# Performance work log

Measured on AMD Instinct MI355X. Metric: run time of the kernel, lower is better.

The kernel has to match this reference:

```python
import jax, jax.numpy as jnp
import numpy as np

LAMBDA_IDENTITY = 1.0
LAMBDA_ATTENTION = 0.5

B, F_FRAMES, N, V = 4, 16, 1024, 4


def setup_inputs() -> dict:
    key = jax.random.key(0)
    k1, k2, k3, k4, k5, k6 = jax.random.split(key, 6)
    refined_points = jax.random.normal(k1, (B, F_FRAMES, N, 3), dtype=jnp.float32)
    gt_points = jax.random.normal(k2, (B, F_FRAMES, N, 3), dtype=jnp.float32)
    visibility = jax.random.randint(k3, (B, F_FRAMES, N), 0, 2, dtype=jnp.int32)
    projection_matrices = jax.random.normal(k4, (V, B, 3, 4), dtype=jnp.float32)
    tracks_2d = jax.random.normal(k5, (V, B, F_FRAMES, N, 2), dtype=jnp.float32)
    correspondence_matrices = jax.random.normal(k6, (V, V, B, N, N), dtype=jnp.float32)
    return {
        'refined_points': refined_points,
        'gt_points': gt_points,
        'visibility': visibility,
        'projection_matrices': projection_matrices,
        'tracks_2d': tracks_2d,
        'correspondence_matrices': correspondence_matrices,
    }


def _reconstruction_loss(pred, gt, visibility):
    mask = (visibility > 0)[..., None]                       # [B,F,N,1]
    se = (pred - gt) ** 2                                    # [B,F,N,3]
    num = jnp.sum(mask) * 3                                  # number of masked scalar elements
    big = jnp.float32(1e30)
    mn = jnp.min(jnp.where(mask, gt, big), axis=(0, 1, 2))   # per-coord min over valid points
    mx = jnp.max(jnp.where(mask, gt, -big), axis=(0, 1, 2))
    scale = jnp.max(mx - mn) + 1e-6
    scale = jnp.where(num > 0, scale, jnp.float32(1.0))
    scale = jax.lax.stop_gradient(scale)
    mse_mean = jnp.sum(jnp.where(mask, se, 0.0)) / jnp.maximum(num, 1)
    return mse_mean / scale ** 2


def _identity_loss(pred, proj, tracks):
    # pred [B,F,N,3], proj [V,B,3,4], tracks [V,B,F,N,2]
    ones = jnp.ones(pred.shape[:-1] + (1,), dtype=pred.dtype)
    homo = jnp.concatenate([pred, ones], axis=-1)            # [B,F,N,4]
    p2h = jnp.einsum('vbij,bfnj->vbfni', proj, homo)         # [V,B,F,N,3]
    p2 = p2h[..., :2] / (p2h[..., 2:3] + 1e-10)              # [V,B,F,N,2]
    valid = jnp.sum(jnp.abs(tracks), axis=-1) > 1e-6         # [V,B,F,N]
    vmask = valid[..., None]
    big = jnp.float32(1e30)
    mn = jnp.min(jnp.where(vmask, tracks, big), axis=3)      # [V,B,F,2]
    mx = jnp.max(jnp.where(vmask, tracks, -big), axis=3)
    wh = jnp.maximum(224.0, mx - mn + 1e-6)                  # (width, height)
    any_valid = jnp.any(valid, axis=3)[..., None]
    wh = jnp.where(any_valid, wh, 224.0)
    wh = jax.lax.stop_gradient(wh)
    err = ((p2 - tracks) / wh[:, :, :, None, :]) ** 2        # [V,B,F,N,2]
    view_loss = jnp.mean(jnp.sum(err, axis=-1), axis=-1)     # [V,B,F]
    return jnp.mean(view_loss)


def _attention_loss(corr, visibility):
    # corr [V,V,B,N,N] logits; visibility [B,F,N]
    n = corr.shape[-1]
    vis = visibility[:, 0, :n] > 0                           # frame 0 visibility [B,N]
    idx = jnp.arange(n)
    d = jnp.abs(idx[:, None] - idx[None, :])
    band = jnp.where(d == 0, 1.0,
           jnp.where(d == 1, 0.7,
           jnp.where(d == 2, 0.49, 0.0))).astype(jnp.float32)   # [N,N]
    pair = jnp.logical_or(vis[:, :, None], vis[:, None, :])     # [B,N,N]
    gt_corr = band[None] * pair.astype(jnp.float32)             # [B,N,N]
    weights = 1.0 + 2.0 * gt_corr
    x = corr
    # stable BCE-with-logits, elementwise weight, mean reduction per matrix
    bce = weights * (jnp.maximum(x, 0.0) - x * gt_corr + jnp.log1p(jnp.exp(-jnp.abs(x))))
    per = jnp.mean(bce, axis=(-1, -2))                          # [V,V,B]
    return jnp.mean(per)                                        # sum / count with count = V*V*B


def reference(refined_points, gt_points, visibility, projection_matrices, tracks_2d, correspondence_matrices):
    rec = _reconstruction_loss(refined_points, gt_points, visibility)
    ident = _identity_loss(refined_points, projection_matrices, tracks_2d)
    att = _attention_loss(correspondence_matrices, visibility)
    total = 1.0 * rec + LAMBDA_IDENTITY * ident + LAMBDA_ATTENTION * att
    return total, rec, ident, att
```

## Files before the change

kernel.cpp:

```cpp
#include <hip/hip_runtime.h>
#include <math.h>

#define B_ 4
#define F_ 16
#define N_ 1024
#define V_ 4


__device__ __forceinline__ unsigned ordEncode(float f) {
    unsigned u = __float_as_uint(f);
    return (u & 0x80000000u) ? ~u : (u | 0x80000000u);
}
__device__ __forceinline__ float ordDecode(unsigned o) {
    unsigned u = (o & 0x80000000u) ? (o & 0x7FFFFFFFu) : ~o;
    return __uint_as_float(u);
}

__global__ void init_ws(double* sums, unsigned* mm) {
    int t = threadIdx.x;
    if (t < 3) sums[t] = 0.0;
    if (t < 7) mm[t] = (t >= 1 && t <= 3) ? 0xFFFFFFFFu : 0u;
}

__global__ __launch_bounds__(256) void rec_kernel(const float* __restrict__ pred,
                                                  const float* __restrict__ gt,
                                                  const int* __restrict__ vis,
                                                  double* sums, unsigned* mm) {
    int p = blockIdx.x * 256 + threadIdx.x;
    bool m = vis[p] > 0;
    float gx = gt[3 * p], gy = gt[3 * p + 1], gz = gt[3 * p + 2];
    float px = pred[3 * p], py = pred[3 * p + 1], pz = pred[3 * p + 2];
    float se = 0.f;
    if (m) {
        float dx = px - gx, dy = py - gy, dz = pz - gz;
        se = dx * dx + dy * dy + dz * dz;
    }
    float mn0 = m ? gx : 1e30f, mn1 = m ? gy : 1e30f, mn2 = m ? gz : 1e30f;
    float mx0 = m ? gx : -1e30f, mx1 = m ? gy : -1e30f, mx2 = m ? gz : -1e30f;
    float c = m ? 1.f : 0.f;
    #pragma unroll
    for (int off = 32; off; off >>= 1) {
        se += __shfl_down(se, off);
        c  += __shfl_down(c, off);
        mn0 = fminf(mn0, __shfl_down(mn0, off));
        mn1 = fminf(mn1, __shfl_down(mn1, off));
        mn2 = fminf(mn2, __shfl_down(mn2, off));
        mx0 = fmaxf(mx0, __shfl_down(mx0, off));
        mx1 = fmaxf(mx1, __shfl_down(mx1, off));
        mx2 = fmaxf(mx2, __shfl_down(mx2, off));
    }
    __shared__ float sh[4][8];
    int wave = threadIdx.x >> 6, lane = threadIdx.x & 63;
    if (lane == 0) {
        sh[wave][0] = se; sh[wave][1] = c;
        sh[wave][2] = mn0; sh[wave][3] = mn1; sh[wave][4] = mn2;
        sh[wave][5] = mx0; sh[wave][6] = mx1; sh[wave][7] = mx2;
    }
    __syncthreads();
    if (threadIdx.x == 0) {
        se = sh[0][0]; c = sh[0][1];
        mn0 = sh[0][2]; mn1 = sh[0][3]; mn2 = sh[0][4];
        mx0 = sh[0][5]; mx1 = sh[0][6]; mx2 = sh[0][7];
        for (int w = 1; w < 4; w++) {
            se += sh[w][0]; c += sh[w][1];
            mn0 = fminf(mn0, sh[w][2]); mn1 = fminf(mn1, sh[w][3]); mn2 = fminf(mn2, sh[w][4]);
            mx0 = fmaxf(mx0, sh[w][5]); mx1 = fmaxf(mx1, sh[w][6]); mx2 = fmaxf(mx2, sh[w][7]);
        }
        atomicAdd(&sums[0], (double)se);
        atomicAdd(&mm[0], (unsigned)(c + 0.5f));
        atomicMin(&mm[1], ordEncode(mn0));
        atomicMin(&mm[2], ordEncode(mn1));
        atomicMin(&mm[3], ordEncode(mn2));
        atomicMax(&mm[4], ordEncode(mx0));
        atomicMax(&mm[5], ordEncode(mx1));
        atomicMax(&mm[6], ordEncode(mx2));
    }
}

__global__ __launch_bounds__(256) void ident_kernel(const float* __restrict__ pred,
                                                    const float* __restrict__ proj,
                                                    const float* __restrict__ tracks,
                                                    double* sums) {
    int idx = blockIdx.x;
    int v = idx / (B_ * F_);
    int b = (idx / F_) % B_;
    int f = idx % F_;
    const float* P = proj + ((size_t)(v * B_ + b)) * 12;
    const float* T = tracks + ((size_t)((v * B_ + b) * F_ + f)) * N_ * 2;
    const float* Q = pred + ((size_t)(b * F_ + f)) * N_ * 3;

    float mnx = 1e30f, mny = 1e30f, mxx = -1e30f, mxy = -1e30f;
    for (int n = threadIdx.x; n < N_; n += 256) {
        float tx = T[2 * n], ty = T[2 * n + 1];
        bool val = (fabsf(tx) + fabsf(ty)) > 1e-6f;
        if (val) {
            mnx = fminf(mnx, tx); mxx = fmaxf(mxx, tx);
            mny = fminf(mny, ty); mxy = fmaxf(mxy, ty);
        }
    }
    #pragma unroll
    for (int off = 32; off; off >>= 1) {
        mnx = fminf(mnx, __shfl_down(mnx, off));
        mxx = fmaxf(mxx, __shfl_down(mxx, off));
        mny = fminf(mny, __shfl_down(mny, off));
        mxy = fmaxf(mxy, __shfl_down(mxy, off));
    }
    __shared__ float sh[4][4];
    __shared__ float wh[2];
    int wave = threadIdx.x >> 6, lane = threadIdx.x & 63;
    if (lane == 0) { sh[wave][0] = mnx; sh[wave][1] = mxx; sh[wave][2] = mny; sh[wave][3] = mxy; }
    __syncthreads();
    if (threadIdx.x == 0) {
        float a = sh[0][0], bb = sh[0][1], c = sh[0][2], d = sh[0][3];
        for (int w = 1; w < 4; w++) {
            a = fminf(a, sh[w][0]); bb = fmaxf(bb, sh[w][1]);
            c = fminf(c, sh[w][2]); d = fmaxf(d, sh[w][3]);
        }
        wh[0] = fmaxf(224.0f, bb - a + 1e-6f);
        wh[1] = fmaxf(224.0f, d - c + 1e-6f);
    }
    __syncthreads();
    float whx = wh[0], why = wh[1];

    float P00 = P[0], P01 = P[1], P02 = P[2], P03 = P[3];
    float P10 = P[4], P11 = P[5], P12 = P[6], P13 = P[7];
    float P20 = P[8], P21 = P[9], P22 = P[10], P23 = P[11];

    float errsum = 0.f;
    for (int n = threadIdx.x; n < N_; n += 256) {
        float x = Q[3 * n], y = Q[3 * n + 1], z = Q[3 * n + 2];
        float p0 = P00 * x + P01 * y + P02 * z + P03;
        float p1 = P10 * x + P11 * y + P12 * z + P13;
        float p2 = P20 * x + P21 * y + P22 * z + P23;
        float den = p2 + 1e-10f;
        float tx = T[2 * n], ty = T[2 * n + 1];
        float ex = (p0 / den - tx) / whx;
        float ey = (p1 / den - ty) / why;
        errsum += ex * ex + ey * ey;
    }
    #pragma unroll
    for (int off = 32; off; off >>= 1) errsum += __shfl_down(errsum, off);
    __shared__ float se2[4];
    if (lane == 0) se2[wave] = errsum;
    __syncthreads();
    if (threadIdx.x == 0) {
        float s = se2[0] + se2[1] + se2[2] + se2[3];
        atomicAdd(&sums[1], (double)(s / (float)N_));
    }
}

__global__ __launch_bounds__(256) void att_kernel(const float* __restrict__ corr,
                                                  const int* __restrict__ vis,
                                                  double* sums) {
    __shared__ unsigned char vs[B_ * N_];
    for (int t = threadIdx.x; t < B_ * N_; t += 256) {
        int b = t >> 10, n = t & (N_ - 1);
        vs[t] = (vis[b * (F_ * N_) + n] > 0) ? 1 : 0;
    }
    __syncthreads();

    const float4* c4 = (const float4*)corr;
    const unsigned total4 = (unsigned)(V_ * V_ * B_) * (unsigned)(N_ * (N_ / 4));
    const unsigned stride = gridDim.x * blockDim.x;
    float acc = 0.f;
    for (unsigned q = blockIdx.x * blockDim.x + threadIdx.x; q < total4; q += stride) {
        float4 x4 = c4[q];
        unsigned base = q * 4u;
        int j0 = (int)(base & (N_ - 1));
        int i  = (int)((base >> 10) & (N_ - 1));
        int b  = (int)((base >> 20) & 3);
        const unsigned char* vrow = &vs[b << 10];
        float vi = (float)vrow[i];
        #pragma unroll
        for (int k = 0; k < 4; k++) {
            float x = (&x4.x)[k];
            int j = j0 + k;
            int d = abs(i - j);
            float band = (d == 0) ? 1.0f : (d == 1) ? 0.7f : (d == 2) ? 0.49f : 0.0f;
            float pair = (vi != 0.f || vrow[j] != 0) ? 1.0f : 0.0f;
            float gt = band * pair;
            float w = 1.0f + 2.0f * gt;
            float ax = fabsf(x);
            float sp = __logf(1.0f + __expf(-ax));
            acc += w * (fmaxf(x, 0.0f) - x * gt + sp);
        }
    }
    #pragma unroll
    for (int off = 32; off; off >>= 1) acc += __shfl_down(acc, off);
    __shared__ float sw[4];
    int wave = threadIdx.x >> 6, lane = threadIdx.x & 63;
    if (lane == 0) sw[wave] = acc;
    __syncthreads();
    if (threadIdx.x == 0) {
        float s = sw[0] + sw[1] + sw[2] + sw[3];
        atomicAdd(&sums[2], (double)s);
    }
}

__global__ void finalize_kernel(const double* sums, const unsigned* mm, float* out) {
    unsigned cnt = mm[0];
    double num = (double)cnt * 3.0;
    double mse = sums[0] / fmax(num, 1.0);
    float rng = -1e30f;
    for (int c = 0; c < 3; c++) {
        float mnv = ordDecode(mm[1 + c]);
        float mxv = ordDecode(mm[4 + c]);
        rng = fmaxf(rng, mxv - mnv);
    }
    float scale = rng + 1e-6f;
    if (cnt == 0) scale = 1.0f;
    float rec = (float)mse / (scale * scale);
    float ident = (float)(sums[1] / (double)(V_ * B_ * F_));
    float att = (float)(sums[2] / ((double)V_ * V_ * B_ * N_ * N_));
    float total = rec + 1.0f * ident + 0.5f * att;
    out[0] = total; out[1] = rec; out[2] = ident; out[3] = att;
}

extern "C" void kernel_launch(void* const* d_in, const int* in_sizes, int n_in,
                              void* d_out, int out_size, void* d_ws, size_t ws_size,
                              hipStream_t stream) {
    const float* refined = (const float*)d_in[0];
    const float* gtp     = (const float*)d_in[1];
    const int*   vis     = (const int*)d_in[2];
    const float* proj    = (const float*)d_in[3];
    const float* tracks  = (const float*)d_in[4];
    const float* corr    = (const float*)d_in[5];
    float* out = (float*)d_out;

    double*   sums = (double*)d_ws;
    unsigned* mm   = (unsigned*)((char*)d_ws + 24);

    init_ws<<<1, 64, 0, stream>>>(sums, mm);
    rec_kernel<<<(B_ * F_ * N_) / 256, 256, 0, stream>>>(refined, gtp, vis, sums, mm);
    ident_kernel<<<V_ * B_ * F_, 256, 0, stream>>>(refined, proj, tracks, sums);
    att_kernel<<<4096, 256, 0, stream>>>(corr, vis, sums);
    finalize_kernel<<<1, 1, 0, stream>>>(sums, mm, out);
}
```

Baseline: 414.8 us.

## Fuse loss kernels into one launch with per-block partials and banded BCE

Merges the reconstruction, identity and attention kernels into a single launch whose blocks branch by index, and replaces the global atomics with per-block partial results reduced by a final 256-thread kernel. This also removes the init kernel. The attention path now computes the BCE algebraically as softplus everywhere plus a correction only near the diagonal band, which skips the per-element weight and pair work. Each block loads one batch's visibility row with a vectorized int4 load, and corr rows are prefetched one iteration ahead. The cost is a larger, more branchy kernel and a workspace layout with fixed offsets.

Result: faster. 376.2 us (-9.3%).

```diff
diff --git a/kernel.cpp b/kernel.cpp
--- a/kernel.cpp
+++ b/kernel.cpp
@@ -6,42 +6,215 @@
 #define N_ 1024
 #define V_ 4
 
-
-__device__ __forceinline__ unsigned ordEncode(float f) {
-    unsigned u = __float_as_uint(f);
-    return (u & 0x80000000u) ? ~u : (u | 0x80000000u);
-}
-__device__ __forceinline__ float ordDecode(unsigned o) {
-    unsigned u = (o & 0x80000000u) ? (o & 0x7FFFFFFFu) : ~o;
-    return __uint_as_float(u);
-}
-
-__global__ void init_ws(double* sums, unsigned* mm) {
-    int t = threadIdx.x;
-    if (t < 3) sums[t] = 0.0;
-    if (t < 7) mm[t] = (t >= 1 && t <= 3) ? 0xFFFFFFFFu : 0u;
-}
-
-__global__ __launch_bounds__(256) void rec_kernel(const float* __restrict__ pred,
-                                                  const float* __restrict__ gt,
-                                                  const int* __restrict__ vis,
-                                                  double* sums, unsigned* mm) {
-    int p = blockIdx.x * 256 + threadIdx.x;
-    bool m = vis[p] > 0;
-    float gx = gt[3 * p], gy = gt[3 * p + 1], gz = gt[3 * p + 2];
-    float px = pred[3 * p], py = pred[3 * p + 1], pz = pred[3 * p + 2];
-    float se = 0.f;
-    if (m) {
-        float dx = px - gx, dy = py - gy, dz = pz - gz;
-        se = dx * dx + dy * dy + dz * dz;
-    }
-    float mn0 = m ? gx : 1e30f, mn1 = m ? gy : 1e30f, mn2 = m ? gz : 1e30f;
-    float mx0 = m ? gx : -1e30f, mx1 = m ? gy : -1e30f, mx2 = m ? gz : -1e30f;
-    float c = m ? 1.f : 0.f;
+#define ATT_BLOCKS 4096
+#define REC_BLOCKS 256
+#define ID_BLOCKS  256
+
+
+__device__ __forceinline__ float softplusf(float x) {
+    float ax = fabsf(x);
+    float e = __expf(-ax);
+    return fmaxf(x, 0.0f) + __logf(1.0f + e);
+}
+
+__global__ __launch_bounds__(256) void mega_kernel(const float* __restrict__ pred,
+                                                   const float* __restrict__ gt,
+                                                   const int* __restrict__ vis,
+                                                   const float* __restrict__ proj,
+                                                   const float* __restrict__ tracks,
+                                                   const float* __restrict__ corr,
+                                                   double* __restrict__ attp,
+                                                   float* __restrict__ recp,
+                                                   float* __restrict__ idp) {
+    const int blk = blockIdx.x;
+    const int t = threadIdx.x;
+    const int wave = t >> 6, lane = t & 63;
+
+    if (blk < ATT_BLOCKS) {
+        const int b = (blk >> 6) & 3;
+        const int row0 = (blk & 63) << 4;
+        __shared__ unsigned char vs[N_];
+        {
+            int4 v4 = ((const int4*)(vis + b * (F_ * N_)))[t];
+            vs[4 * t + 0] = v4.x > 0;
+            vs[4 * t + 1] = v4.y > 0;
+            vs[4 * t + 2] = v4.z > 0;
+            vs[4 * t + 3] = v4.w > 0;
+        }
+        __syncthreads();
+
+        const float4* base4 = (const float4*)corr + (size_t)blk * 4096;
+        const int j0 = 4 * t;
+        float acc = 0.f;
+        float4 cur = base4[t];
+        #pragma unroll
+        for (int k = 0; k < 16; k++) {
+            float4 nxt = cur;
+            if (k < 15) nxt = base4[(k + 1) * 256 + t];
+            const int i = row0 + k;
+            float x0 = cur.x, x1 = cur.y, x2 = cur.z, x3 = cur.w;
+            float sp0 = softplusf(x0), sp1 = softplusf(x1);
+            float sp2 = softplusf(x2), sp3 = softplusf(x3);
+            acc += (sp0 + sp1) + (sp2 + sp3);
+            if (j0 >= i - 5 && j0 <= i + 2) {
+                float xs[4] = {x0, x1, x2, x3};
+                float sps[4] = {sp0, sp1, sp2, sp3};
+                unsigned char vi = vs[i];
+                #pragma unroll
+                for (int kk = 0; kk < 4; kk++) {
+                    int j = j0 + kk;
+                    int d = (i > j) ? (i - j) : (j - i);
+                    if (d <= 2) {
+                        if (vi | vs[j]) {
+                            float g = (d == 0) ? 1.0f : ((d == 1) ? 0.7f : 0.49f);
+                            acc += 2.f * g * sps[kk] - (1.f + 2.f * g) * xs[kk] * g;
+                        }
+                    }
+                }
+            }
+            cur = nxt;
+        }
+        #pragma unroll
+        for (int off = 32; off; off >>= 1) acc += __shfl_down(acc, off);
+        __shared__ double sw[4];
+        if (lane == 0) sw[wave] = (double)acc;
+        __syncthreads();
+        if (t == 0) attp[blk] = (sw[0] + sw[1]) + (sw[2] + sw[3]);
+
+    } else if (blk < ATT_BLOCKS + REC_BLOCKS) {
+        const int r = blk - ATT_BLOCKS;
+        const int p = r * 256 + t;
+        bool m = vis[p] > 0;
+        float gx = gt[3 * p], gy = gt[3 * p + 1], gz = gt[3 * p + 2];
+        float px = pred[3 * p], py = pred[3 * p + 1], pz = pred[3 * p + 2];
+        float se = 0.f;
+        if (m) {
+            float dx = px - gx, dy = py - gy, dz = pz - gz;
+            se = dx * dx + dy * dy + dz * dz;
+        }
+        float mn0 = m ? gx : 1e30f, mn1 = m ? gy : 1e30f, mn2 = m ? gz : 1e30f;
+        float mx0 = m ? gx : -1e30f, mx1 = m ? gy : -1e30f, mx2 = m ? gz : -1e30f;
+        float c = m ? 1.f : 0.f;
+        #pragma unroll
+        for (int off = 32; off; off >>= 1) {
+            se += __shfl_down(se, off);
+            c  += __shfl_down(c, off);
+            mn0 = fminf(mn0, __shfl_down(mn0, off));
+            mn1 = fminf(mn1, __shfl_down(mn1, off));
+            mn2 = fminf(mn2, __shfl_down(mn2, off));
+            mx0 = fmaxf(mx0, __shfl_down(mx0, off));
+            mx1 = fmaxf(mx1, __shfl_down(mx1, off));
+            mx2 = fmaxf(mx2, __shfl_down(mx2, off));
+        }
+        __shared__ float sh[4][8];
+        if (lane == 0) {
+            sh[wave][0] = se; sh[wave][1] = c;
+            sh[wave][2] = mn0; sh[wave][3] = mn1; sh[wave][4] = mn2;
+            sh[wave][5] = mx0; sh[wave][6] = mx1; sh[wave][7] = mx2;
+        }
+        __syncthreads();
+        if (t == 0) {
+            se = sh[0][0]; c = sh[0][1];
+            mn0 = sh[0][2]; mn1 = sh[0][3]; mn2 = sh[0][4];
+            mx0 = sh[0][5]; mx1 = sh[0][6]; mx2 = sh[0][7];
+            for (int w = 1; w < 4; w++) {
+                se += sh[w][0]; c += sh[w][1];
+                mn0 = fminf(mn0, sh[w][2]); mn1 = fminf(mn1, sh[w][3]); mn2 = fminf(mn2, sh[w][4]);
+                mx0 = fmaxf(mx0, sh[w][5]); mx1 = fmaxf(mx1, sh[w][6]); mx2 = fmaxf(mx2, sh[w][7]);
+            }
+            float* o = recp + r * 8;
+            o[0] = se; o[1] = c;
+            o[2] = mn0; o[3] = mn1; o[4] = mn2;
+            o[5] = mx0; o[6] = mx1; o[7] = mx2;
+        }
+
+    } else {
+        const int idx = blk - (ATT_BLOCKS + REC_BLOCKS);
+        const int v = idx / (B_ * F_);
+        const int b = (idx / F_) % B_;
+        const int f = idx % F_;
+        const float* P = proj + ((size_t)(v * B_ + b)) * 12;
+        const float* T = tracks + ((size_t)((v * B_ + b) * F_ + f)) * N_ * 2;
+        const float* Q = pred + ((size_t)(b * F_ + f)) * N_ * 3;
+
+        float mnx = 1e30f, mny = 1e30f, mxx = -1e30f, mxy = -1e30f;
+        for (int n = t; n < N_; n += 256) {
+            float tx = T[2 * n], ty = T[2 * n + 1];
+            if ((fabsf(tx) + fabsf(ty)) > 1e-6f) {
+                mnx = fminf(mnx, tx); mxx = fmaxf(mxx, tx);
+                mny = fminf(mny, ty); mxy = fmaxf(mxy, ty);
+            }
+        }
+        #pragma unroll
+        for (int off = 32; off; off >>= 1) {
+            mnx = fminf(mnx, __shfl_down(mnx, off));
+            mxx = fmaxf(mxx, __shfl_down(mxx, off));
+            mny = fminf(mny, __shfl_down(mny, off));
+            mxy = fmaxf(mxy, __shfl_down(mxy, off));
+        }
+        __shared__ float shi[4][4];
+        __shared__ float wh[2];
+        if (lane == 0) { shi[wave][0] = mnx; shi[wave][1] = mxx; shi[wave][2] = mny; shi[wave][3] = mxy; }
+        __syncthreads();
+        if (t == 0) {
+            float a = shi[0][0], bb = shi[0][1], c = shi[0][2], d = shi[0][3];
+            for (int w = 1; w < 4; w++) {
+                a = fminf(a, shi[w][0]); bb = fmaxf(bb, shi[w][1]);
+                c = fminf(c, shi[w][2]); d = fmaxf(d, shi[w][3]);
+            }
+            wh[0] = fmaxf(224.0f, bb - a + 1e-6f);
+            wh[1] = fmaxf(224.0f, d - c + 1e-6f);
+        }
+        __syncthreads();
+        float whx = wh[0], why = wh[1];
+
+        float P00 = P[0], P01 = P[1], P02 = P[2], P03 = P[3];
+        float P10 = P[4], P11 = P[5], P12 = P[6], P13 = P[7];
+        float P20 = P[8], P21 = P[9], P22 = P[10], P23 = P[11];
+
+        float errsum = 0.f;
+        for (int n = t; n < N_; n += 256) {
+            float x = Q[3 * n], y = Q[3 * n + 1], z = Q[3 * n + 2];
+            float p0 = P00 * x + P01 * y + P02 * z + P03;
+            float p1 = P10 * x + P11 * y + P12 * z + P13;
+            float p2 = P20 * x + P21 * y + P22 * z + P23;
+            float den = p2 + 1e-10f;
+            float tx = T[2 * n], ty = T[2 * n + 1];
+            float ex = (p0 / den - tx) / whx;
+            float ey = (p1 / den - ty) / why;
+            errsum += ex * ex + ey * ey;
+        }
+        #pragma unroll
+        for (int off = 32; off; off >>= 1) errsum += __shfl_down(errsum, off);
+        __shared__ float se2[4];
+        if (lane == 0) se2[wave] = errsum;
+        __syncthreads();
+        if (t == 0) idp[idx] = (se2[0] + se2[1] + se2[2] + se2[3]) / (float)N_;
+    }
+}
+
+__global__ __launch_bounds__(256) void fin_kernel(const double* __restrict__ attp,
+                                                  const float* __restrict__ recp,
+                                                  const float* __restrict__ idp,
+                                                  float* __restrict__ out) {
+    const int t = threadIdx.x;
+    const int wave = t >> 6, lane = t & 63;
+
+    double a = 0.0;
+    for (int k = t; k < ATT_BLOCKS; k += 256) a += attp[k];
+    const float* rp = recp + t * 8;
+    double se = (double)rp[0];
+    double c  = (double)rp[1];
+    float mn0 = rp[2], mn1 = rp[3], mn2 = rp[4];
+    float mx0 = rp[5], mx1 = rp[6], mx2 = rp[7];
+    double id = (double)idp[t];
+
     #pragma unroll
     for (int off = 32; off; off >>= 1) {
+        a  += __shfl_down(a, off);
         se += __shfl_down(se, off);
         c  += __shfl_down(c, off);
+        id += __shfl_down(id, off);
         mn0 = fminf(mn0, __shfl_down(mn0, off));
         mn1 = fminf(mn1, __shfl_down(mn1, off));
         mn2 = fminf(mn2, __shfl_down(mn2, off));
@@ -49,171 +222,34 @@
         mx1 = fmaxf(mx1, __shfl_down(mx1, off));
         mx2 = fmaxf(mx2, __shfl_down(mx2, off));
     }
-    __shared__ float sh[4][8];
-    int wave = threadIdx.x >> 6, lane = threadIdx.x & 63;
+    __shared__ double sa[4], sse[4], sc[4], sid[4];
+    __shared__ float smn[3][4], smx[3][4];
     if (lane == 0) {
-        sh[wave][0] = se; sh[wave][1] = c;
-        sh[wave][2] = mn0; sh[wave][3] = mn1; sh[wave][4] = mn2;
-        sh[wave][5] = mx0; sh[wave][6] = mx1; sh[wave][7] = mx2;
+        sa[wave] = a; sse[wave] = se; sc[wave] = c; sid[wave] = id;
+        smn[0][wave] = mn0; smn[1][wave] = mn1; smn[2][wave] = mn2;
+        smx[0][wave] = mx0; smx[1][wave] = mx1; smx[2][wave] = mx2;
     }
     __syncthreads();
-    if (threadIdx.x == 0) {
-        se = sh[0][0]; c = sh[0][1];
-        mn0 = sh[0][2]; mn1 = sh[0][3]; mn2 = sh[0][4];
-        mx0 = sh[0][5]; mx1 = sh[0][6]; mx2 = sh[0][7];
+    if (t == 0) {
+        a = sa[0]; se = sse[0]; c = sc[0]; id = sid[0];
+        mn0 = smn[0][0]; mn1 = smn[1][0]; mn2 = smn[2][0];
+        mx0 = smx[0][0]; mx1 = smx[1][0]; mx2 = smx[2][0];
         for (int w = 1; w < 4; w++) {
-            se += sh[w][0]; c += sh[w][1];
-            mn0 = fminf(mn0, sh[w][2]); mn1 = fminf(mn1, sh[w][3]); mn2 = fminf(mn2, sh[w][4]);
-            mx0 = fmaxf(mx0, sh[w][5]); mx1 = fmaxf(mx1, sh[w][6]); mx2 = fmaxf(mx2, sh[w][7]);
-        }
-        atomicAdd(&sums[0], (double)se);
-        atomicAdd(&mm[0], (unsigned)(c + 0.5f));
-        atomicMin(&mm[1], ordEncode(mn0));
-        atomicMin(&mm[2], ordEncode(mn1));
-        atomicMin(&mm[3], ordEncode(mn2));
-        atomicMax(&mm[4], ordEncode(mx0));
-        atomicMax(&mm[5], ordEncode(mx1));
-        atomicMax(&mm[6], ordEncode(mx2));
-    }
-}
-
-__global__ __launch_bounds__(256) void ident_kernel(const float* __restrict__ pred,
-                                                    const float* __restrict__ proj,
-                                                    const float* __restrict__ tracks,
-                                                    double* sums) {
-    int idx = blockIdx.x;
-    int v = idx / (B_ * F_);
-    int b = (idx / F_) % B_;
-    int f = idx % F_;
-    const float* P = proj + ((size_t)(v * B_ + b)) * 12;
-    const float* T = tracks + ((size_t)((v * B_ + b) * F_ + f)) * N_ * 2;
-    const float* Q = pred + ((size_t)(b * F_ + f)) * N_ * 3;
-
-    float mnx = 1e30f, mny = 1e30f, mxx = -1e30f, mxy = -1e30f;
-    for (int n = threadIdx.x; n < N_; n += 256) {
-        float tx = T[2 * n], ty = T[2 * n + 1];
-        bool val = (fabsf(tx) + fabsf(ty)) > 1e-6f;
-        if (val) {
-            mnx = fminf(mnx, tx); mxx = fmaxf(mxx, tx);
-            mny = fminf(mny, ty); mxy = fmaxf(mxy, ty);
-        }
-    }
-    #pragma unroll
-    for (int off = 32; off; off >>= 1) {
-        mnx = fminf(mnx, __shfl_down(mnx, off));
-        mxx = fmaxf(mxx, __shfl_down(mxx, off));
-        mny = fminf(mny, __shfl_down(mny, off));
-        mxy = fmaxf(mxy, __shfl_down(mxy, off));
-    }
-    __shared__ float sh[4][4];
-    __shared__ float wh[2];
-    int wave = threadIdx.x >> 6, lane = threadIdx.x & 63;
-    if (lane == 0) { sh[wave][0] = mnx; sh[wave][1] = mxx; sh[wave][2] = mny; sh[wave][3] = mxy; }
-    __syncthreads();
-    if (threadIdx.x == 0) {
-        float a = sh[0][0], bb = sh[0][1], c = sh[0][2], d = sh[0][3];
-        for (int w = 1; w < 4; w++) {
-            a = fminf(a, sh[w][0]); bb = fmaxf(bb, sh[w][1]);
-            c = fminf(c, sh[w][2]); d = fmaxf(d, sh[w][3]);
-        }
-        wh[0] = fmaxf(224.0f, bb - a + 1e-6f);
-        wh[1] = fmaxf(224.0f, d - c + 1e-6f);
-    }
-    __syncthreads();
-    float whx = wh[0], why = wh[1];
-
-    float P00 = P[0], P01 = P[1], P02 = P[2], P03 = P[3];
-    float P10 = P[4], P11 = P[5], P12 = P[6], P13 = P[7];
-    float P20 = P[8], P21 = P[9], P22 = P[10], P23 = P[11];
-
-    float errsum = 0.f;
-    for (int n = threadIdx.x; n < N_; n += 256) {
-        float x = Q[3 * n], y = Q[3 * n + 1], z = Q[3 * n + 2];
-        float p0 = P00 * x + P01 * y + P02 * z + P03;
-        float p1 = P10 * x + P11 * y + P12 * z + P13;
-        float p2 = P20 * x + P21 * y + P22 * z + P23;
-        float den = p2 + 1e-10f;
-        float tx = T[2 * n], ty = T[2 * n + 1];
-        float ex = (p0 / den - tx) / whx;
-        float ey = (p1 / den - ty) / why;
-        errsum += ex * ex + ey * ey;
-    }
-    #pragma unroll
-    for (int off = 32; off; off >>= 1) errsum += __shfl_down(errsum, off);
-    __shared__ float se2[4];
-    if (lane == 0) se2[wave] = errsum;
-    __syncthreads();
-    if (threadIdx.x == 0) {
-        float s = se2[0] + se2[1] + se2[2] + se2[3];
-        atomicAdd(&sums[1], (double)(s / (float)N_));
-    }
-}
-
-__global__ __launch_bounds__(256) void att_kernel(const float* __restrict__ corr,
-                                                  const int* __restrict__ vis,
-                                                  double* sums) {
-    __shared__ unsigned char vs[B_ * N_];
-    for (int t = threadIdx.x; t < B_ * N_; t += 256) {
-        int b = t >> 10, n = t & (N_ - 1);
-        vs[t] = (vis[b * (F_ * N_) + n] > 0) ? 1 : 0;
-    }
-    __syncthreads();
-
-    const float4* c4 = (const float4*)corr;
-    const unsigned total4 = (unsigned)(V_ * V_ * B_) * (unsigned)(N_ * (N_ / 4));
-    const unsigned stride = gridDim.x * blockDim.x;
-    float acc = 0.f;
-    for (unsigned q = blockIdx.x * blockDim.x + threadIdx.x; q < total4; q += stride) {
-        float4 x4 = c4[q];
-        unsigned base = q * 4u;
-        int j0 = (int)(base & (N_ - 1));
-        int i  = (int)((base >> 10) & (N_ - 1));
-        int b  = (int)((base >> 20) & 3);
-        const unsigned char* vrow = &vs[b << 10];
-        float vi = (float)vrow[i];
-        #pragma unroll
-        for (int k = 0; k < 4; k++) {
-            float x = (&x4.x)[k];
-            int j = j0 + k;
-            int d = abs(i - j);
-            float band = (d == 0) ? 1.0f : (d == 1) ? 0.7f : (d == 2) ? 0.49f : 0.0f;
-            float pair = (vi != 0.f || vrow[j] != 0) ? 1.0f : 0.0f;
-            float gt = band * pair;
-            float w = 1.0f + 2.0f * gt;
-            float ax = fabsf(x);
-            float sp = __logf(1.0f + __expf(-ax));
-            acc += w * (fmaxf(x, 0.0f) - x * gt + sp);
-        }
-    }
-    #pragma unroll
-    for (int off = 32; off; off >>= 1) acc += __shfl_down(acc, off);
-    __shared__ float sw[4];
-    int wave = threadIdx.x >> 6, lane = threadIdx.x & 63;
-    if (lane == 0) sw[wave] = acc;
-    __syncthreads();
-    if (threadIdx.x == 0) {
-        float s = sw[0] + sw[1] + sw[2] + sw[3];
-        atomicAdd(&sums[2], (double)s);
-    }
-}
-
-__global__ void finalize_kernel(const double* sums, const unsigned* mm, float* out) {
-    unsigned cnt = mm[0];
-    double num = (double)cnt * 3.0;
-    double mse = sums[0] / fmax(num, 1.0);
-    float rng = -1e30f;
-    for (int c = 0; c < 3; c++) {
-        float mnv = ordDecode(mm[1 + c]);
-        float mxv = ordDecode(mm[4 + c]);
-        rng = fmaxf(rng, mxv - mnv);
-    }
-    float scale = rng + 1e-6f;
-    if (cnt == 0) scale = 1.0f;
-    float rec = (float)mse / (scale * scale);
-    float ident = (float)(sums[1] / (double)(V_ * B_ * F_));
-    float att = (float)(sums[2] / ((double)V_ * V_ * B_ * N_ * N_));
-    float total = rec + 1.0f * ident + 0.5f * att;
-    out[0] = total; out[1] = rec; out[2] = ident; out[3] = att;
+            a += sa[w]; se += sse[w]; c += sc[w]; id += sid[w];
+            mn0 = fminf(mn0, smn[0][w]); mn1 = fminf(mn1, smn[1][w]); mn2 = fminf(mn2, smn[2][w]);
+            mx0 = fmaxf(mx0, smx[0][w]); mx1 = fmaxf(mx1, smx[1][w]); mx2 = fmaxf(mx2, smx[2][w]);
+        }
+        double num = c * 3.0;
+        double mse = se / fmax(num, 1.0);
+        float rng = fmaxf(mx0 - mn0, fmaxf(mx1 - mn1, mx2 - mn2));
+        float scale = rng + 1e-6f;
+        if (c < 0.5) scale = 1.0f;
+        float rec = (float)mse / (scale * scale);
+        float ident = (float)(id / (double)(V_ * B_ * F_));
+        float att = (float)(a / ((double)V_ * V_ * B_ * N_ * N_));
+        float total = rec + 1.0f * ident + 0.5f * att;
+        out[0] = total; out[1] = rec; out[2] = ident; out[3] = att;
+    }
 }
 
 extern "C" void kernel_launch(void* const* d_in, const int* in_sizes, int n_in,
@@ -227,12 +263,11 @@
     const float* corr    = (const float*)d_in[5];
     float* out = (float*)d_out;
 
-    double*   sums = (double*)d_ws;
-    unsigned* mm   = (unsigned*)((char*)d_ws + 24);
-
-    init_ws<<<1, 64, 0, stream>>>(sums, mm);
-    rec_kernel<<<(B_ * F_ * N_) / 256, 256, 0, stream>>>(refined, gtp, vis, sums, mm);
-    ident_kernel<<<V_ * B_ * F_, 256, 0, stream>>>(refined, proj, tracks, sums);
-    att_kernel<<<4096, 256, 0, stream>>>(corr, vis, sums);
-    finalize_kernel<<<1, 1, 0, stream>>>(sums, mm, out);
-}
+    double* attp = (double*)d_ws;
+    float*  recp = (float*)((char*)d_ws + 32768);
+    float*  idp  = (float*)((char*)d_ws + 40960);
+
+    mega_kernel<<<ATT_BLOCKS + REC_BLOCKS + ID_BLOCKS, 256, 0, stream>>>(
+        refined, gtp, vis, proj, tracks, corr, attp, recp, idp);
+    fin_kernel<<<1, 256, 0, stream>>>(attp, recp, idp, out);
+}
```
